# Kernel tuning notes

Hardware: AMD Instinct MI355X
Metric: run time of the kernel (lower is better)

The kernel has to match this reference:

```python
import jax, jax.numpy as jnp
import numpy as np

NTOKEN, NINP, NHID, NLAYERS = 32000, 1024, 1024, 2
SEQ, BATCH = 128, 32


def setup_inputs() -> dict:
    key = jax.random.key(0)
    ks = jax.random.split(key, 6)
    initrange = 0.1
    tokens = jax.random.randint(ks[0], (SEQ, BATCH), 0, NTOKEN)
    h0 = jnp.zeros((NLAYERS, BATCH, NHID), jnp.float32)
    c0 = jnp.zeros((NLAYERS, BATCH, NHID), jnp.float32)
    emb_table = jax.random.uniform(ks[1], (NTOKEN, NINP), jnp.float32, -initrange, initrange)
    # nn.Linear(2H, 4H): weight [4H, 2H]; store transposed [2H, 4H] for x @ W
    lstm_W = jax.random.normal(ks[2], (NLAYERS, 2 * NHID, 4 * NHID), jnp.float32) * (1.0 / np.sqrt(2 * NHID))
    lstm_b = jax.random.normal(ks[3], (NLAYERS, 4 * NHID), jnp.float32) * 0.01
    dec_W = jax.random.uniform(ks[4], (NHID, NTOKEN), jnp.float32, -initrange, initrange)
    dec_b = jnp.zeros((NTOKEN,), jnp.float32)
    return {"tokens": tokens, "h0": h0, "c0": c0, "emb_table": emb_table,
            "lstm_W": lstm_W, "lstm_b": lstm_b, "dec_W": dec_W, "dec_b": dec_b}


def _lstm_scan(emb, h0, c0, lstm_W, lstm_b):
    def step(carry, x_t):  # x_t: [B, H]
        h, c = carry  # each [L, B, H]
        hs, cs = [], []
        inp = x_t
        for l in range(NLAYERS):
            gates = jnp.concatenate([inp, h[l]], axis=1) @ lstm_W[l] + lstm_b[l]  # [B, 4H]
            i, j, f, o = jnp.split(gates, 4, axis=1)
            c_new = c[l] * jax.nn.sigmoid(f) + jax.nn.sigmoid(i) * jnp.tanh(j)
            h_new = jnp.tanh(c_new) * jax.nn.sigmoid(o)
            hs.append(h_new)
            cs.append(c_new)
            inp = h_new
        return (jnp.stack(hs), jnp.stack(cs)), inp

    (h_last, c_last), outputs = jax.lax.scan(step, (h0, c0), emb)
    return outputs, h_last, c_last  # outputs: [S, B, H]


def reference(tokens, h0, c0, emb_table, lstm_W, lstm_b, dec_W, dec_b):
    emb = emb_table[tokens]  # [S, B, NINP]
    outputs, h_last, c_last = _lstm_scan(emb, h0, c0, lstm_W, lstm_b)
    decoded = outputs @ dec_W + dec_b  # [S, B, NTOKEN]
    return decoded, (h_last, c_last)
```

## Files before the change

### kernel.cpp

```cpp
#include <hip/hip_runtime.h>

typedef __attribute__((ext_vector_type(8))) short bf16x8;
typedef __attribute__((ext_vector_type(4))) float f32x4;
typedef const __attribute__((address_space(1))) void* gas_ptr;
typedef __attribute__((address_space(3))) void* las_ptr;

__device__ __forceinline__ unsigned short f2bf(float f) {
  unsigned int u = __float_as_uint(f);
  return (unsigned short)((u + 0x7fffu + ((u >> 16) & 1u)) >> 16);
}
__device__ __forceinline__ unsigned int cvt_pk_bf16(float a, float b) {
  unsigned int r;
  asm volatile("v_cvt_pk_bf16_f32 %0, %1, %2" : "=v"(r) : "v"(a), "v"(b));
  return r;
}
__device__ __forceinline__ float sigm(float x) { return 1.0f / (1.0f + __expf(-x)); }

__device__ __forceinline__ void st_cv(unsigned int* p, unsigned int v) {
  __hip_atomic_store(p, v, __ATOMIC_RELAXED, __HIP_MEMORY_SCOPE_AGENT);
}

__device__ __forceinline__ void gbarF(int* bars, int target, int bid) {
  __syncthreads();
  if (threadIdx.x == 0) {
    int* leaf  = bars + (bid & 15) * 32;
    int* mcnt  = bars + 512;
    int* sense = bars + 640;
    if (__hip_atomic_fetch_add(leaf, 1, __ATOMIC_RELAXED, __HIP_MEMORY_SCOPE_AGENT) == 15) {
      __hip_atomic_store(leaf, 0, __ATOMIC_RELAXED, __HIP_MEMORY_SCOPE_AGENT);
      if (__hip_atomic_fetch_add(mcnt, 1, __ATOMIC_RELAXED, __HIP_MEMORY_SCOPE_AGENT) == 15) {
        __hip_atomic_store(mcnt, 0, __ATOMIC_RELAXED, __HIP_MEMORY_SCOPE_AGENT);
        __hip_atomic_store(sense, target, __ATOMIC_RELAXED, __HIP_MEMORY_SCOPE_AGENT);
      }
    }
    while (__hip_atomic_load(sense, __ATOMIC_RELAXED, __HIP_MEMORY_SCOPE_AGENT) < target)
      __builtin_amdgcn_s_sleep(1);
  }
  __syncthreads();
}

__global__ __launch_bounds__(256) void init_kernel(
    const float* __restrict__ h0_in,
    unsigned short* __restrict__ h0buf, unsigned short* __restrict__ h1buf,
    int* __restrict__ bar)
{
  const int j = blockIdx.x * 256 + threadIdx.x;
  if (j < 768) bar[j] = 0;
  h0buf[j] = f2bf(h0_in[j]);
  h1buf[32768 + j] = f2bf(h0_in[32768 + j]);
}

__global__ __launch_bounds__(256) void gather_emb(
    const int* __restrict__ tokens, const float* __restrict__ etab,
    unsigned short* __restrict__ xemb)
{
  const int r = blockIdx.x;
  const float* src = etab + (size_t)tokens[r] * 1024;
  const int q = threadIdx.x * 4;
  const float4 v = *(const float4*)(src + q);
  uint2 o;
  o.x = cvt_pk_bf16(v.x, v.y);
  o.y = cvt_pk_bf16(v.z, v.w);
  *(uint2*)(xemb + (size_t)r * 1024 + q) = o;
}

__global__ __launch_bounds__(256) void reorg_lstm_w(
    const float* __restrict__ W, char* __restrict__ wimg)
{
  __shared__ float tile[64 * 36];
  const int bid = blockIdx.x;
  const int layer = bid >> 7;
  const int u0 = (bid & 127) * 8;
  const int tid = threadIdx.x;
  const float* Wl = W + (size_t)layer * 2048 * 4096;
  char* img = wimg + (size_t)bid * 131072;
  const int kl = tid >> 2, g = tid & 3;
  const int row = tid & 15, ksub = (tid >> 4) & 3;
  const int tn = (tid >> 6) & 1, kl2 = tid >> 7;
  const int c = tn * 16 + row;
#pragma unroll 1
  for (int kt = 0; kt < 32; ++kt) {
    const float* src = Wl + (size_t)(kt * 64 + kl) * 4096 + g * 1024 + u0;
    const float4 v0 = *(const float4*)src;
    const float4 v1 = *(const float4*)(src + 4);
    *(float4*)(tile + kl * 36 + g * 8) = v0;
    *(float4*)(tile + kl * 36 + g * 8 + 4) = v1;
    __syncthreads();
    const int kbase = kl2 * 32 + ksub * 8;
    uint4 u;
    u.x = cvt_pk_bf16(tile[(kbase + 0) * 36 + c], tile[(kbase + 1) * 36 + c]);
    u.y = cvt_pk_bf16(tile[(kbase + 2) * 36 + c], tile[(kbase + 3) * 36 + c]);
    u.z = cvt_pk_bf16(tile[(kbase + 4) * 36 + c], tile[(kbase + 5) * 36 + c]);
    u.w = cvt_pk_bf16(tile[(kbase + 6) * 36 + c], tile[(kbase + 7) * 36 + c]);
    const int S = (kt * 2 + kl2) * 128 + tn * 64 + ksub * 16 + row;
    *(uint4*)(img + (size_t)S * 16) = u;
    __syncthreads();
  }
}

__global__ __launch_bounds__(512, 1) void lstm_seq_kernel(
    const char* __restrict__ wimg, const float* __restrict__ bias,
    const float* __restrict__ c0_in,
    const unsigned short* __restrict__ xemb,
    unsigned short* __restrict__ h0buf, unsigned short* __restrict__ h1buf,
    unsigned short* __restrict__ hseq,
    float* __restrict__ out_tail, int* __restrict__ bar)
{
  __shared__ __align__(16) char smem[148608];
  char* wlds   = smem;
  float* red   = (float*)(smem + 131072);
  float* gates = (float*)(smem + 143360);
  float* cl    = (float*)(smem + 147584);

  const int tid = threadIdx.x;
  const int bid = blockIdx.x;
  const int layer = bid >> 7;
  const int u0 = (bid & 127) * 8;
  const int lane = tid & 63, w = tid >> 6;
  const int tb = w & 1, kq = w >> 1;
  const int row = tb * 16 + (lane & 15);
  const int kg = lane >> 4;
  unsigned short* hmy = layer ? h1buf : h0buf;

  {
    const char* img = wimg + (size_t)bid * 131072;
#pragma unroll 1
    for (int i = 0; i < 16; ++i) {
      const int off = (i * 512 + tid) * 16;
      __builtin_amdgcn_global_load_lds((gas_ptr)(img + off), (las_ptr)(wlds + off), 16, 0, 0);
    }
    if (tid < 256) cl[tid] = c0_in[layer * 32768 + (tid >> 3) * 1024 + u0 + (tid & 7)];
  }
  const int cc = lane & 15;
  const float biasv0 = bias[layer * 4096 + (cc >> 3) * 1024 + u0 + (cc & 7)];
  const float biasv1 = bias[layer * 4096 + ((cc + 16) >> 3) * 1024 + u0 + (cc & 7)];
  asm volatile("s_waitcnt vmcnt(0)");
  __syncthreads();

  const char* wq = wlds + (size_t)(kq * 16 * 128 + lane) * 16;

  for (int p = 0; p <= 128; ++p) {
    const bool active = layer ? (p >= 1) : (p < 128);
    if (active) {
      const int t = layer ? (p - 1) : p;
      const char* xb;
      bool coh;
      if (kq < 2) {
        if (layer == 0) {
          xb = (const char*)xemb + (size_t)t * 65536 + row * 2048 + (kq & 1) * 1024 + kg * 16;
          coh = false;
        } else {
          xb = (const char*)h0buf + (p & 1) * 65536 + row * 2048 + (kq & 1) * 1024 + kg * 16;
          coh = true;
        }
      } else {
        xb = (const char*)hmy + (p & 1) * 65536 + row * 2048 + (kq & 1) * 1024 + kg * 16;
        coh = true;
      }

      bf16x8 a[16];
      if (!coh) {
#pragma unroll
        for (int j = 0; j < 16; ++j) a[j] = *(const bf16x8*)(xb + j * 64);
      } else {
#pragma unroll
        for (int j = 0; j < 16; ++j)
          asm volatile("global_load_dwordx4 %0, %1, off sc0 sc1"
                       : "=v"(a[j]) : "v"(xb + j * 64) : "memory");
        asm volatile("s_waitcnt vmcnt(0)" ::: "memory");
        __builtin_amdgcn_sched_barrier(0);
      }

      f32x4 acc0 = {0.f, 0.f, 0.f, 0.f}, acc1 = {0.f, 0.f, 0.f, 0.f};
#pragma unroll
      for (int j = 0; j < 16; ++j) {
        const bf16x8 b0 = *(const bf16x8*)(wq + (size_t)j * 2048);
        const bf16x8 b1 = *(const bf16x8*)(wq + (size_t)j * 2048 + 1024);
        acc0 = __builtin_amdgcn_mfma_f32_16x16x32_bf16(a[j], b0, acc0, 0, 0, 0);
        acc1 = __builtin_amdgcn_mfma_f32_16x16x32_bf16(a[j], b1, acc1, 0, 0, 0);
      }

      if (kq > 0) {
        const int s0 = (((kq - 1) * 2 + tb) * 2 + 0) * 64 + lane;
        const int s1 = (((kq - 1) * 2 + tb) * 2 + 1) * 64 + lane;
        *(f32x4*)(red + s0 * 4) = acc0;
        *(f32x4*)(red + s1 * 4) = acc1;
      }
      __syncthreads();
      if (kq == 0) {
#pragma unroll
        for (int q = 1; q < 4; ++q) {
          const f32x4 o0 = *(const f32x4*)(red + ((((q - 1) * 2 + tb) * 2 + 0) * 64 + lane) * 4);
          const f32x4 o1 = *(const f32x4*)(red + ((((q - 1) * 2 + tb) * 2 + 1) * 64 + lane) * 4);
#pragma unroll
          for (int r = 0; r < 4; ++r) { acc0[r] += o0[r]; acc1[r] += o1[r]; }
        }
        const int rb = tb * 16 + kg * 4;
#pragma unroll
        for (int r = 0; r < 4; ++r) {
          gates[(rb + r) * 33 + cc] = acc0[r] + biasv0;
          gates[(rb + r) * 33 + 16 + cc] = acc1[r] + biasv1;
        }
      }
      __syncthreads();
      if (tid < 128) {
        const int cb = tid >> 2, up = (tid & 3) * 2;
        const float gi0 = gates[cb * 33 + up],      gi1 = gates[cb * 33 + up + 1];
        const float gj0 = gates[cb * 33 + 8 + up],  gj1 = gates[cb * 33 + 9 + up];
        const float gf0 = gates[cb * 33 + 16 + up], gf1 = gates[cb * 33 + 17 + up];
        const float go0 = gates[cb * 33 + 24 + up], go1 = gates[cb * 33 + 25 + up];
        const float cn0 = cl[cb * 8 + up] * sigm(gf0) + sigm(gi0) * tanhf(gj0);
        const float cn1 = cl[cb * 8 + up + 1] * sigm(gf1) + sigm(gi1) * tanhf(gj1);
        const float hn0 = tanhf(cn0) * sigm(go0);
        const float hn1 = tanhf(cn1) * sigm(go1);
        cl[cb * 8 + up] = cn0;
        cl[cb * 8 + up + 1] = cn1;
        const unsigned int pk = cvt_pk_bf16(hn0, hn1);
        st_cv((unsigned int*)(hmy + ((p + 1) & 1) * 32768 + cb * 1024 + u0 + up), pk);
        if (layer) *(unsigned int*)(hseq + (size_t)t * 32768 + cb * 1024 + u0 + up) = pk;
        if (t == 127) {
          float* ot = out_tail + layer * 32768 + cb * 1024 + u0 + up;
          ot[0] = hn0; ot[1] = hn1;
          ot[65536] = cn0; ot[65537] = cn1;
        }
      }
    }
    if (p < 128) gbarF(bar, p + 1, bid);
  }
}

__global__ __launch_bounds__(256) void transpose_decw_kernel(
    const float* __restrict__ decW, unsigned short* __restrict__ Wt)
{
  __shared__ float tile[64 * 68];
  const int bid = blockIdx.x;
  const int k0 = (bid & 15) * 64;
  const int n0 = (bid >> 4) * 64;
  const int tid = threadIdx.x;
  {
    const int kl = tid >> 4, c4 = (tid & 15) * 4;
#pragma unroll
    for (int i = 0; i < 4; ++i) {
      const int kr = kl + 16 * i;
      *(float4*)(tile + kr * 68 + c4) =
          *(const float4*)(decW + (size_t)(k0 + kr) * 32000 + n0 + c4);
    }
  }
  __syncthreads();
  {
    const int nl = tid >> 3, kc = (tid & 7) * 8;
#pragma unroll
    for (int h2 = 0; h2 < 2; ++h2) {
      const int n = nl + 32 * h2;
      float tv[8];
#pragma unroll
      for (int q = 0; q < 8; ++q) tv[q] = tile[(kc + q) * 68 + n];
      uint4 u;
      u.x = cvt_pk_bf16(tv[0], tv[1]);
      u.y = cvt_pk_bf16(tv[2], tv[3]);
      u.z = cvt_pk_bf16(tv[4], tv[5]);
      u.w = cvt_pk_bf16(tv[6], tv[7]);
      *(uint4*)(Wt + (size_t)(n0 + n) * 1024 + k0 + kc) = u;
    }
  }
}

__global__ __launch_bounds__(256) void decoder_kernel(
    const unsigned short* __restrict__ A,
    const unsigned short* __restrict__ Bt,
    const float* __restrict__ decb,
    float* __restrict__ out)
{
  __shared__ unsigned short Al[2][128 * 32];
  __shared__ unsigned short Bl[2][128 * 32];

  const int bid = blockIdx.x;
  const int swz = (bid & 7) * 1000 + (bid >> 3);
  const int mt = swz / 250, nt = swz % 250;
  const int m0 = mt * 128, n0 = nt * 128;

  const int tid = threadIdx.x;
  const int lane = tid & 63;
  const int wv = tid >> 6;
  const int wr = wv >> 1, wc = wv & 1;
  const int l15 = lane & 15, kg = lane >> 4;

  f32x4 acc[4][4];
#pragma unroll
  for (int mi = 0; mi < 4; ++mi)
#pragma unroll
    for (int ni = 0; ni < 4; ++ni) {
      f32x4 z = {0.f, 0.f, 0.f, 0.f};
      acc[mi][ni] = z;
    }

  auto stage = [&](const unsigned short* src, int row0, int k0, unsigned short* lds) {
#pragma unroll
    for (int j = 0; j < 2; ++j) {
      const int chunk = (wv * 2 + j) * 64 + lane;
      const int r = chunk >> 2, kc = chunk & 3;
      const unsigned short* g = src + (size_t)(row0 + r) * 1024 + k0 + kc * 8;
      __builtin_amdgcn_global_load_lds((gas_ptr)g, (las_ptr)(lds + chunk * 8), 16, 0, 0);
    }
  };

  stage(A, m0, 0, Al[0]);
  stage(Bt, n0, 0, Bl[0]);
  __syncthreads();

  int buf = 0;
  for (int kt = 0; kt < 32; ++kt) {
    if (kt < 31) {
      stage(A, m0, (kt + 1) * 32, Al[buf ^ 1]);
      stage(Bt, n0, (kt + 1) * 32, Bl[buf ^ 1]);
    }
    bf16x8 a[4], b[4];
#pragma unroll
    for (int mi = 0; mi < 4; ++mi)
      a[mi] = *(const bf16x8*)&Al[buf][(wr * 64 + mi * 16 + l15) * 32 + kg * 8];
#pragma unroll
    for (int ni = 0; ni < 4; ++ni)
      b[ni] = *(const bf16x8*)&Bl[buf][(wc * 64 + ni * 16 + l15) * 32 + kg * 8];
#pragma unroll
    for (int mi = 0; mi < 4; ++mi)
#pragma unroll
      for (int ni = 0; ni < 4; ++ni)
        acc[mi][ni] = __builtin_amdgcn_mfma_f32_16x16x32_bf16(a[mi], b[ni], acc[mi][ni], 0, 0, 0);
    __syncthreads();
    buf ^= 1;
  }

#pragma unroll
  for (int ni = 0; ni < 4; ++ni) {
    const int ocol = n0 + wc * 64 + ni * 16 + l15;
    const float bv = decb[ocol];
#pragma unroll
    for (int mi = 0; mi < 4; ++mi) {
      const int orow = m0 + wr * 64 + mi * 16 + kg * 4;
#pragma unroll
      for (int r = 0; r < 4; ++r)
        out[(size_t)(orow + r) * 32000 + ocol] = acc[mi][ni][r] + bv;
    }
  }
}

extern "C" void kernel_launch(void* const* d_in, const int* in_sizes, int n_in,
                              void* d_out, int out_size, void* d_ws, size_t ws_size,
                              hipStream_t stream) {
  (void)in_sizes; (void)n_in; (void)out_size; (void)ws_size;
  const int* tokens  = (const int*)d_in[0];
  const float* h0_in = (const float*)d_in[1];
  const float* c0_in = (const float*)d_in[2];
  const float* etab  = (const float*)d_in[3];
  const float* lstmW = (const float*)d_in[4];
  const float* lstmb = (const float*)d_in[5];
  const float* decW  = (const float*)d_in[6];
  const float* decb  = (const float*)d_in[7];
  float* out = (float*)d_out;

  char* ws = (char*)d_ws;
  unsigned short* hseq  = (unsigned short*)(ws + 0);
  char* img             = ws + 8388608;
  unsigned short* Wt    = (unsigned short*)(ws + 8388608);
  unsigned short* xemb  = (unsigned short*)(ws + 41943040);
  unsigned short* h0buf = (unsigned short*)(ws + 73924608);
  unsigned short* h1buf = (unsigned short*)(ws + 74055680);
  int* bar              = (int*)(ws + 74186752);

  init_kernel<<<128, 256, 0, stream>>>(h0_in, h0buf, h1buf, bar);
  gather_emb<<<4096, 256, 0, stream>>>(tokens, etab, xemb);
  reorg_lstm_w<<<256, 256, 0, stream>>>(lstmW, img);
  lstm_seq_kernel<<<256, 512, 0, stream>>>(img, lstmb, c0_in, xemb,
                                           h0buf, h1buf, hseq,
                                           out + 131072000, bar);
  transpose_decw_kernel<<<8000, 256, 0, stream>>>(decW, Wt);
  decoder_kernel<<<8000, 256, 0, stream>>>(hseq, Wt, decb, out);
}
```

Measured before the change: 1.387 ms.

## Replace tree grid barrier with striped counters and prefetch embeddings across steps

Replaces the two-level sense-reversal grid barrier with eight monotonically increasing counters. Each block bumps one counter with a single atomic, and every thread polls all eight with two coherent vector loads until each reaches 32 times the step. This is meant to cut barrier latency on each of the 129 recurrent steps. Layer-0 input waves now prefetch the next step's embedding rows into registers before the poll, so that load overlaps the barrier wait. The recurrent-h loads are consumed in four staged waitcnt groups, letting MFMAs start before all sixteen loads land. The cost is heavier polling traffic from all threads and relaxed-ordering correctness that depends on the coherent loads and stores.

```diff
diff --git a/kernel.cpp b/kernel.cpp
--- a/kernel.cpp
+++ b/kernel.cpp
@@ -2,6 +2,7 @@
 
 typedef __attribute__((ext_vector_type(8))) short bf16x8;
 typedef __attribute__((ext_vector_type(4))) float f32x4;
+typedef __attribute__((ext_vector_type(4))) unsigned int u32x4;
 typedef const __attribute__((address_space(1))) void* gas_ptr;
 typedef __attribute__((address_space(3))) void* las_ptr;
 
@@ -15,28 +16,10 @@
   return r;
 }
 __device__ __forceinline__ float sigm(float x) { return 1.0f / (1.0f + __expf(-x)); }
+__device__ __forceinline__ unsigned umin2(unsigned a, unsigned b) { return a < b ? a : b; }
 
 __device__ __forceinline__ void st_cv(unsigned int* p, unsigned int v) {
   __hip_atomic_store(p, v, __ATOMIC_RELAXED, __HIP_MEMORY_SCOPE_AGENT);
-}
-
-__device__ __forceinline__ void gbarF(int* bars, int target, int bid) {
-  __syncthreads();
-  if (threadIdx.x == 0) {
-    int* leaf  = bars + (bid & 15) * 32;
-    int* mcnt  = bars + 512;
-    int* sense = bars + 640;
-    if (__hip_atomic_fetch_add(leaf, 1, __ATOMIC_RELAXED, __HIP_MEMORY_SCOPE_AGENT) == 15) {
-      __hip_atomic_store(leaf, 0, __ATOMIC_RELAXED, __HIP_MEMORY_SCOPE_AGENT);
-      if (__hip_atomic_fetch_add(mcnt, 1, __ATOMIC_RELAXED, __HIP_MEMORY_SCOPE_AGENT) == 15) {
-        __hip_atomic_store(mcnt, 0, __ATOMIC_RELAXED, __HIP_MEMORY_SCOPE_AGENT);
-        __hip_atomic_store(sense, target, __ATOMIC_RELAXED, __HIP_MEMORY_SCOPE_AGENT);
-      }
-    }
-    while (__hip_atomic_load(sense, __ATOMIC_RELAXED, __HIP_MEMORY_SCOPE_AGENT) < target)
-      __builtin_amdgcn_s_sleep(1);
-  }
-  __syncthreads();
 }
 
 __global__ __launch_bounds__(256) void init_kernel(
@@ -121,6 +104,8 @@
   const int row = tb * 16 + (lane & 15);
   const int kg = lane >> 4;
   unsigned short* hmy = layer ? h1buf : h0buf;
+  unsigned* barp = (unsigned*)bar;
+  const bool statx = (layer == 0) && (kq < 2);
 
   {
     const char* img = wimg + (size_t)bid * 131072;
@@ -139,45 +124,66 @@
 
   const char* wq = wlds + (size_t)(kq * 16 * 128 + lane) * 16;
 
+  bf16x8 a[16];
+  if (statx) {
+    const char* xn = (const char*)xemb + row * 2048 + kq * 1024 + kg * 16;
+#pragma unroll
+    for (int j = 0; j < 16; ++j) a[j] = *(const bf16x8*)(xn + j * 64);
+  }
+
   for (int p = 0; p <= 128; ++p) {
+    if (p > 0) {
+      const unsigned tgt = 32u * (unsigned)p;
+      while (true) {
+        u32x4 c0, c1;
+        asm volatile(
+            "global_load_dwordx4 %0, %2, off sc0 sc1\n\t"
+            "global_load_dwordx4 %1, %2, off offset:16 sc0 sc1\n\t"
+            "s_waitcnt vmcnt(0)"
+            : "=v"(c0), "=v"(c1) : "v"(barp) : "memory");
+        const unsigned m = umin2(umin2(umin2(c0[0], c0[1]), umin2(c0[2], c0[3])),
+                                 umin2(umin2(c1[0], c1[1]), umin2(c1[2], c1[3])));
+        if (m >= tgt) break;
+        __builtin_amdgcn_s_sleep(1);
+      }
+    }
+
     const bool active = layer ? (p >= 1) : (p < 128);
     if (active) {
       const int t = layer ? (p - 1) : p;
-      const char* xb;
-      bool coh;
-      if (kq < 2) {
-        if (layer == 0) {
-          xb = (const char*)xemb + (size_t)t * 65536 + row * 2048 + (kq & 1) * 1024 + kg * 16;
-          coh = false;
-        } else {
-          xb = (const char*)h0buf + (p & 1) * 65536 + row * 2048 + (kq & 1) * 1024 + kg * 16;
-          coh = true;
-        }
-      } else {
-        xb = (const char*)hmy + (p & 1) * 65536 + row * 2048 + (kq & 1) * 1024 + kg * 16;
-        coh = true;
-      }
-
-      bf16x8 a[16];
-      if (!coh) {
-#pragma unroll
-        for (int j = 0; j < 16; ++j) a[j] = *(const bf16x8*)(xb + j * 64);
-      } else {
+      f32x4 acc0 = {0.f, 0.f, 0.f, 0.f}, acc1 = {0.f, 0.f, 0.f, 0.f};
+
+      if (!statx) {
+        const char* src = (layer && kq < 2) ? (const char*)h0buf : (const char*)hmy;
+        const char* xb = src + (p & 1) * 65536 + row * 2048 + (kq & 1) * 1024 + kg * 16;
 #pragma unroll
         for (int j = 0; j < 16; ++j)
           asm volatile("global_load_dwordx4 %0, %1, off sc0 sc1"
                        : "=v"(a[j]) : "v"(xb + j * 64) : "memory");
-        asm volatile("s_waitcnt vmcnt(0)" ::: "memory");
-        __builtin_amdgcn_sched_barrier(0);
-      }
-
-      f32x4 acc0 = {0.f, 0.f, 0.f, 0.f}, acc1 = {0.f, 0.f, 0.f, 0.f};
-#pragma unroll
-      for (int j = 0; j < 16; ++j) {
-        const bf16x8 b0 = *(const bf16x8*)(wq + (size_t)j * 2048);
-        const bf16x8 b1 = *(const bf16x8*)(wq + (size_t)j * 2048 + 1024);
-        acc0 = __builtin_amdgcn_mfma_f32_16x16x32_bf16(a[j], b0, acc0, 0, 0, 0);
-        acc1 = __builtin_amdgcn_mfma_f32_16x16x32_bf16(a[j], b1, acc1, 0, 0, 0);
+#pragma unroll
+        for (int g = 0; g < 4; ++g) {
+          asm volatile("s_waitcnt vmcnt(%0)" :: "n"(12 - 4 * 0) : "memory");
+          if (g == 0) asm volatile("s_waitcnt vmcnt(12)" ::: "memory");
+          else if (g == 1) asm volatile("s_waitcnt vmcnt(8)" ::: "memory");
+          else if (g == 2) asm volatile("s_waitcnt vmcnt(4)" ::: "memory");
+          else asm volatile("s_waitcnt vmcnt(0)" ::: "memory");
+          __builtin_amdgcn_sched_barrier(0);
+#pragma unroll
+          for (int j = g * 4; j < g * 4 + 4; ++j) {
+            const bf16x8 b0 = *(const bf16x8*)(wq + (size_t)j * 2048);
+            const bf16x8 b1 = *(const bf16x8*)(wq + (size_t)j * 2048 + 1024);
+            acc0 = __builtin_amdgcn_mfma_f32_16x16x32_bf16(a[j], b0, acc0, 0, 0, 0);
+            acc1 = __builtin_amdgcn_mfma_f32_16x16x32_bf16(a[j], b1, acc1, 0, 0, 0);
+          }
+        }
+      } else {
+#pragma unroll
+        for (int j = 0; j < 16; ++j) {
+          const bf16x8 b0 = *(const bf16x8*)(wq + (size_t)j * 2048);
+          const bf16x8 b1 = *(const bf16x8*)(wq + (size_t)j * 2048 + 1024);
+          acc0 = __builtin_amdgcn_mfma_f32_16x16x32_bf16(a[j], b0, acc0, 0, 0, 0);
+          acc1 = __builtin_amdgcn_mfma_f32_16x16x32_bf16(a[j], b1, acc1, 0, 0, 0);
+        }
       }
 
       if (kq > 0) {
@@ -225,7 +231,17 @@
         }
       }
     }
-    if (p < 128) gbarF(bar, p + 1, bid);
+
+    if (p < 128) {
+      __syncthreads();
+      if (tid == 0)
+        __hip_atomic_fetch_add(barp + (bid & 7), 1u, __ATOMIC_RELAXED, __HIP_MEMORY_SCOPE_AGENT);
+      if (statx && (p + 1) < 128) {
+        const char* xn = (const char*)xemb + (size_t)(p + 1) * 65536 + row * 2048 + kq * 1024 + kg * 16;
+#pragma unroll
+        for (int j = 0; j < 16; ++j) a[j] = *(const bf16x8*)(xn + j * 64);
+      }
+    }
   }
 }
 
```

Measured after the change: 2.183 ms. 57.4% more time.

## Split grid barrier into arrive/wait and prefetch next embedding during wait

Applied to the files above, without the earlier changes.

The global barrier is split into separate arrive and wait phases. Layer-0 waves that read static embedding input now prefetch the next timestep's embedding rows into registers between arrive and wait, so that load is hidden behind barrier latency. For the coherent h-state loads, the MFMA chain is staged with partial vmcnt waits so compute starts on early chunks while later loads are still in flight. This holds the A-operand registers live across iterations, which raises register pressure.

```diff
diff --git a/kernel.cpp b/kernel.cpp
--- a/kernel.cpp
+++ b/kernel.cpp
@@ -20,23 +20,22 @@
   __hip_atomic_store(p, v, __ATOMIC_RELAXED, __HIP_MEMORY_SCOPE_AGENT);
 }
 
-__device__ __forceinline__ void gbarF(int* bars, int target, int bid) {
-  __syncthreads();
-  if (threadIdx.x == 0) {
-    int* leaf  = bars + (bid & 15) * 32;
-    int* mcnt  = bars + 512;
-    int* sense = bars + 640;
-    if (__hip_atomic_fetch_add(leaf, 1, __ATOMIC_RELAXED, __HIP_MEMORY_SCOPE_AGENT) == 15) {
-      __hip_atomic_store(leaf, 0, __ATOMIC_RELAXED, __HIP_MEMORY_SCOPE_AGENT);
-      if (__hip_atomic_fetch_add(mcnt, 1, __ATOMIC_RELAXED, __HIP_MEMORY_SCOPE_AGENT) == 15) {
-        __hip_atomic_store(mcnt, 0, __ATOMIC_RELAXED, __HIP_MEMORY_SCOPE_AGENT);
-        __hip_atomic_store(sense, target, __ATOMIC_RELAXED, __HIP_MEMORY_SCOPE_AGENT);
-      }
-    }
-    while (__hip_atomic_load(sense, __ATOMIC_RELAXED, __HIP_MEMORY_SCOPE_AGENT) < target)
-      __builtin_amdgcn_s_sleep(1);
-  }
-  __syncthreads();
+__device__ __forceinline__ void gbar_arrive(int* bars, int target, int bid) {
+  int* leaf  = bars + (bid & 15) * 32;
+  int* mcnt  = bars + 512;
+  int* sense = bars + 640;
+  if (__hip_atomic_fetch_add(leaf, 1, __ATOMIC_RELAXED, __HIP_MEMORY_SCOPE_AGENT) == 15) {
+    __hip_atomic_store(leaf, 0, __ATOMIC_RELAXED, __HIP_MEMORY_SCOPE_AGENT);
+    if (__hip_atomic_fetch_add(mcnt, 1, __ATOMIC_RELAXED, __HIP_MEMORY_SCOPE_AGENT) == 15) {
+      __hip_atomic_store(mcnt, 0, __ATOMIC_RELAXED, __HIP_MEMORY_SCOPE_AGENT);
+      __hip_atomic_store(sense, target, __ATOMIC_RELAXED, __HIP_MEMORY_SCOPE_AGENT);
+    }
+  }
+}
+__device__ __forceinline__ void gbar_wait(int* bars, int target) {
+  int* sense = bars + 640;
+  while (__hip_atomic_load(sense, __ATOMIC_RELAXED, __HIP_MEMORY_SCOPE_AGENT) < target)
+    __builtin_amdgcn_s_sleep(1);
 }
 
 __global__ __launch_bounds__(256) void init_kernel(
@@ -121,6 +120,7 @@
   const int row = tb * 16 + (lane & 15);
   const int kg = lane >> 4;
   unsigned short* hmy = layer ? h1buf : h0buf;
+  const bool statx = (layer == 0) && (kq < 2);
 
   {
     const char* img = wimg + (size_t)bid * 131072;
@@ -139,45 +139,55 @@
 
   const char* wq = wlds + (size_t)(kq * 16 * 128 + lane) * 16;
 
+  bf16x8 a[16];
+  if (statx) {
+    const char* xn = (const char*)xemb + row * 2048 + kq * 1024 + kg * 16;
+#pragma unroll
+    for (int j = 0; j < 16; ++j) a[j] = *(const bf16x8*)(xn + j * 64);
+  }
+
   for (int p = 0; p <= 128; ++p) {
     const bool active = layer ? (p >= 1) : (p < 128);
     if (active) {
       const int t = layer ? (p - 1) : p;
-      const char* xb;
-      bool coh;
-      if (kq < 2) {
-        if (layer == 0) {
-          xb = (const char*)xemb + (size_t)t * 65536 + row * 2048 + (kq & 1) * 1024 + kg * 16;
-          coh = false;
-        } else {
-          xb = (const char*)h0buf + (p & 1) * 65536 + row * 2048 + (kq & 1) * 1024 + kg * 16;
-          coh = true;
-        }
-      } else {
-        xb = (const char*)hmy + (p & 1) * 65536 + row * 2048 + (kq & 1) * 1024 + kg * 16;
-        coh = true;
-      }
-
-      bf16x8 a[16];
-      if (!coh) {
-#pragma unroll
-        for (int j = 0; j < 16; ++j) a[j] = *(const bf16x8*)(xb + j * 64);
-      } else {
+      f32x4 acc0 = {0.f, 0.f, 0.f, 0.f}, acc1 = {0.f, 0.f, 0.f, 0.f};
+
+      if (!statx) {
+        const char* src = (layer && kq < 2) ? (const char*)h0buf : (const char*)hmy;
+        const char* xb = src + (p & 1) * 65536 + row * 2048 + (kq & 1) * 1024 + kg * 16;
 #pragma unroll
         for (int j = 0; j < 16; ++j)
           asm volatile("global_load_dwordx4 %0, %1, off sc0 sc1"
                        : "=v"(a[j]) : "v"(xb + j * 64) : "memory");
+        auto mm4 = [&](int j0) {
+#pragma unroll
+          for (int j = j0; j < j0 + 4; ++j) {
+            const bf16x8 b0 = *(const bf16x8*)(wq + (size_t)j * 2048);
+            const bf16x8 b1 = *(const bf16x8*)(wq + (size_t)j * 2048 + 1024);
+            acc0 = __builtin_amdgcn_mfma_f32_16x16x32_bf16(a[j], b0, acc0, 0, 0, 0);
+            acc1 = __builtin_amdgcn_mfma_f32_16x16x32_bf16(a[j], b1, acc1, 0, 0, 0);
+          }
+        };
+        asm volatile("s_waitcnt vmcnt(12)" ::: "memory");
+        __builtin_amdgcn_sched_barrier(0);
+        mm4(0);
+        asm volatile("s_waitcnt vmcnt(8)" ::: "memory");
+        __builtin_amdgcn_sched_barrier(0);
+        mm4(4);
+        asm volatile("s_waitcnt vmcnt(4)" ::: "memory");
+        __builtin_amdgcn_sched_barrier(0);
+        mm4(8);
         asm volatile("s_waitcnt vmcnt(0)" ::: "memory");
         __builtin_amdgcn_sched_barrier(0);
-      }
-
-      f32x4 acc0 = {0.f, 0.f, 0.f, 0.f}, acc1 = {0.f, 0.f, 0.f, 0.f};
-#pragma unroll
-      for (int j = 0; j < 16; ++j) {
-        const bf16x8 b0 = *(const bf16x8*)(wq + (size_t)j * 2048);
-        const bf16x8 b1 = *(const bf16x8*)(wq + (size_t)j * 2048 + 1024);
-        acc0 = __builtin_amdgcn_mfma_f32_16x16x32_bf16(a[j], b0, acc0, 0, 0, 0);
-        acc1 = __builtin_amdgcn_mfma_f32_16x16x32_bf16(a[j], b1, acc1, 0, 0, 0);
+        mm4(12);
+      } else {
+#pragma unroll
+        for (int j = 0; j < 16; ++j) {
+          const bf16x8 b0 = *(const bf16x8*)(wq + (size_t)j * 2048);
+          const bf16x8 b1 = *(const bf16x8*)(wq + (size_t)j * 2048 + 1024);
+          acc0 = __builtin_amdgcn_mfma_f32_16x16x32_bf16(a[j], b0, acc0, 0, 0, 0);
+          acc1 = __builtin_amdgcn_mfma_f32_16x16x32_bf16(a[j], b1, acc1, 0, 0, 0);
+        }
       }
 
       if (kq > 0) {
@@ -225,7 +235,18 @@
         }
       }
     }
-    if (p < 128) gbarF(bar, p + 1, bid);
+
+    if (p < 128) {
+      __syncthreads();
+      if (tid == 0) gbar_arrive(bar, p + 1, bid);
+      if (statx && (p + 1) < 128) {
+        const char* xn = (const char*)xemb + (size_t)(p + 1) * 65536 + row * 2048 + kq * 1024 + kg * 16;
+#pragma unroll
+        for (int j = 0; j < 16; ++j) a[j] = *(const bf16x8*)(xn + j * 64);
+      }
+      if (tid == 0) gbar_wait(bar, p + 1);
+      __syncthreads();
+    }
   }
 }
 
```

Result: no change. 1.362 ms (-1.8%).
